# Kernel optimization log

Hardware: AMD Instinct MI355X
Metric: run time of the kernel (lower is better)

## Reference

```python
import jax, jax.numpy as jnp
import numpy as np

B, N, D = 8, 1024, 256
H = 8
DH = D // H
R = 4          # relation types 0..3; adj value 4 = no relation
FF = 1024
EPS = 1e-5


def _lin(k, fan_in, shape):
    return jax.random.normal(k, shape, jnp.float32) * (1.0 / np.sqrt(fan_in))


def setup_inputs() -> dict:
    key = jax.random.key(0)
    ks = jax.random.split(key, 16)
    src = jax.random.normal(ks[0], (B, N, D), jnp.float32)
    adj_matrix = jax.random.randint(ks[1], (B, N, N), 0, 5, dtype=jnp.int32)
    Wq = _lin(ks[2], D, (D, D)); bq = jnp.zeros((D,), jnp.float32)
    Wk = _lin(ks[3], D, (D, D)); bk = jnp.zeros((D,), jnp.float32)
    Wv = _lin(ks[4], D, (R, D, D)); bv = jnp.zeros((R, D), jnp.float32)
    Wo = _lin(ks[5], D, (D, D)); bo = jnp.zeros((D,), jnp.float32)
    W1 = _lin(ks[6], D, (D, FF)); b1 = jnp.zeros((FF,), jnp.float32)
    W2 = _lin(ks[7], FF, (FF, D)); b2 = jnp.zeros((D,), jnp.float32)
    g1 = jnp.ones((D,), jnp.float32); beta1 = jnp.zeros((D,), jnp.float32)
    g2 = jnp.ones((D,), jnp.float32); beta2 = jnp.zeros((D,), jnp.float32)
    return dict(src=src, adj_matrix=adj_matrix, Wq=Wq, bq=bq, Wk=Wk, bk=bk,
                Wv=Wv, bv=bv, Wo=Wo, bo=bo, W1=W1, b1=b1, W2=W2, b2=b2,
                g1=g1, beta1=beta1, g2=g2, beta2=beta2)


def _ln(x, g, b):
    m = x.mean(-1, keepdims=True)
    v = ((x - m) ** 2).mean(-1, keepdims=True)
    return (x - m) * jax.lax.rsqrt(v + EPS) * g + b


def reference(src, adj_matrix, Wq, bq, Wk, bk, Wv, bv, Wo, bo, W1, b1, W2, b2, g1, beta1, g2, beta2):
    Bb, Nn, Dm = src.shape
    h, dh = H, Dm // H
    q = (src @ Wq + bq).reshape(Bb, Nn, h, dh).transpose(0, 2, 1, 3)  # (B,H,N,dh)
    k = (src @ Wk + bk).reshape(Bb, Nn, h, dh).transpose(0, 2, 1, 3)
    scores = jnp.einsum('bhid,bhjd->bhij', q, k) / np.sqrt(dh)
    attn = jax.nn.softmax(scores, axis=-1)                             # (B,H,N,N)
    out = jnp.zeros_like(q)
    for r in range(Wv.shape[0]):  # small fixed relation loop, matches module
        v_r = (src @ Wv[r] + bv[r]).reshape(Bb, Nn, h, dh).transpose(0, 2, 1, 3)
        mask = (adj_matrix == r)[:, None]                              # (B,1,N,N)
        out = out + jnp.einsum('bhij,bhjd->bhid', attn * mask, v_r)
    attn_out = out.transpose(0, 2, 1, 3).reshape(Bb, Nn, Dm) @ Wo + bo
    x = _ln(src + attn_out, g1, beta1)
    ff = jax.nn.gelu(x @ W1 + b1, approximate=False) @ W2 + b2
    return _ln(x + ff, g2, beta2)
```

## Files before the change

### kernel.cpp

```cpp
#include <hip/hip_runtime.h>
#include <hip/hip_bf16.h>
#include <cmath>

constexpr int CB  = 8;
constexpr int CN  = 1024;
constexpr int CD  = 256;
constexpr int CH  = 8;
constexpr int CDH = 32;
constexpr int CR  = 4;
constexpr int CFF = 1024;
constexpr float CEPS = 1e-5f;
constexpr float CS = 0.25503480f;
constexpr size_t SZH = (size_t)CB * CH * CN * CDH;

#define MODE_QK    0
#define MODE_FFN1  2
#define MODE_VT    4

typedef float v4f __attribute__((ext_vector_type(4)));
typedef short v8s __attribute__((ext_vector_type(8)));

static __device__ __forceinline__ short f2bf(float f) {
    unsigned u = __builtin_bit_cast(unsigned, f);
    u += 0x7fff + ((u >> 16) & 1);
    return (short)(u >> 16);
}
static __device__ __forceinline__ float bf2f(short s) {
    unsigned u = ((unsigned)(unsigned short)s) << 16;
    return __builtin_bit_cast(float, u);
}
static __device__ __forceinline__ unsigned cvtpk_bf16(float lo, float hi) {
    unsigned r;
    asm("v_cvt_pk_bf16_f32 %0, %1, %2" : "=v"(r) : "v"(lo), "v"(hi));
    return r;
}

static __device__ __forceinline__ void async_copy16(const void* g, void* l) {
    __builtin_amdgcn_global_load_lds(
        (const __attribute__((address_space(1))) void*)g,
        (__attribute__((address_space(3))) void*)l, 16, 0, 0);
}


template<int BM, int BN, int MODE>
__device__ __forceinline__ void gemm_body(
    const short* __restrict__ A, const short* __restrict__ Bw,
    const float* __restrict__ biasv, void* __restrict__ dest,
    int M, int K, int Nw, int bx, int by, short* smem)
{
    constexpr int WTM = BM / 2, WTN = BN / 2;
    constexpr int TM = WTM / 16, TN = WTN / 16;
    short* As = smem;
    short* Bs = smem + 2 * BM * 32;

    const int t    = threadIdx.x;
    const int lane = t & 63;
    const int w    = t >> 6;
    const int quad = lane >> 4, l15 = lane & 15;
    const int wm = w >> 1, wn = w & 1;
    const int m0 = bx * BM, n0 = by * BN;

    const int srow = lane >> 2;
    const int scol = (lane & 3) * 8;

    v4f acc[TM][TN];
    #pragma unroll
    for (int i = 0; i < TM; ++i)
        #pragma unroll
        for (int j = 0; j < TN; ++j) acc[i][j] = (v4f){0.f, 0.f, 0.f, 0.f};

    const int NK = K >> 5;

    auto stage = [&](int buf, int kt) {
        #pragma unroll
        for (int u = 0; u < BM / 64; ++u) {
            const int e0 = (w * (BM / 64) + u) * 512;
            const int row = (e0 >> 5) + srow;
            async_copy16(A + (size_t)(m0 + row) * K + kt + scol,
                         &As[buf * BM * 32 + e0]);
        }
        #pragma unroll
        for (int u = 0; u < BN / 64; ++u) {
            const int e0 = (w * (BN / 64) + u) * 512;
            const int row = (e0 >> 5) + srow;
            async_copy16(Bw + (size_t)(n0 + row) * K + kt + scol,
                         &Bs[buf * BN * 32 + e0]);
        }
    };

    stage(0, 0);

    for (int it = 0; it < NK; ++it) {
        __syncthreads();
        if (it + 1 < NK) stage((it + 1) & 1, (it + 1) << 5);

        const int buf = it & 1;
        v8s af[TM], bfr[TN];
        #pragma unroll
        for (int i = 0; i < TM; ++i)
            af[i] = *(const v8s*)&As[buf * BM * 32 +
                                     (wm * WTM + i * 16 + l15) * 32 + quad * 8];
        #pragma unroll
        for (int j = 0; j < TN; ++j)
            bfr[j] = *(const v8s*)&Bs[buf * BN * 32 +
                                      (wn * WTN + j * 16 + l15) * 32 + quad * 8];
        #pragma unroll
        for (int i = 0; i < TM; ++i)
            #pragma unroll
            for (int j = 0; j < TN; ++j)
                acc[i][j] = __builtin_amdgcn_mfma_f32_16x16x32_bf16(
                    af[i], bfr[j], acc[i][j], 0, 0, 0);
    }

    #pragma unroll
    for (int i = 0; i < TM; ++i) {
        #pragma unroll
        for (int j = 0; j < TN; ++j) {
            const int mb = m0 + wm * WTM + i * 16 + quad * 4;
            const int n  = n0 + wn * WTN + j * 16 + l15;
            float vals[4];
            if (MODE == MODE_VT) {
                #pragma unroll
                for (int rr = 0; rr < 4; ++rr) vals[rr] = acc[i][j][rr] + biasv[mb + rr];
            } else {
                #pragma unroll
                for (int rr = 0; rr < 4; ++rr) vals[rr] = acc[i][j][rr] + biasv[n];
            }

            if (MODE == MODE_QK) {
                if (n0 < 256) {
                    #pragma unroll
                    for (int rr = 0; rr < 4; ++rr) vals[rr] *= CS;
                }
                const int b = mb >> 10, ii0 = mb & 1023;
                const int plane = n >> 8, nn = n & 255;
                const int h = nn >> 5, d = nn & 31;
                #pragma unroll
                for (int rr = 0; rr < 4; ++rr)
                    ((short*)dest)[(size_t)plane * SZH +
                        (((size_t)(b * CH + h)) * CN + ii0 + rr) * CDH + d] =
                        f2bf(vals[rr]);
            } else if (MODE == MODE_VT) {
                const int b = n >> 10, ii = n & 1023;
                const int jj = ii & 63;
                const int cc = (((jj >> 4) & 1) << 5) | (((jj >> 2) & 3) << 3) |
                               (((jj >> 5) & 1) << 2) | (jj & 3);
                const int iip = (ii & ~63) | cc;
                #pragma unroll
                for (int rr = 0; rr < 4; ++rr) {
                    const int m = mb + rr;
                    const int r2 = m >> 8, hd = m & 255;
                    const int h = hd >> 5, d = hd & 31;
                    ((short*)dest)[2 * SZH +
                        (((size_t)(r2 * 64 + b * CH + h)) * CDH + d) * CN + iip] =
                        f2bf(vals[rr]);
                }
            } else {
                #pragma unroll
                for (int rr = 0; rr < 4; ++rr) {
                    const size_t idx = (size_t)(mb + rr) * Nw + n;
                    const float xx = vals[rr];
                    const float E = exp2f(2.302217f * (xx + 0.044715f * xx * xx * xx));
                    ((short*)dest)[idx] = f2bf(xx * E / (E + 1.f));
                }
            }
        }
    }
}

template<int BM, int BN, int MODE>
__global__ __launch_bounds__(256)
void gemm_mfma(const short* __restrict__ A, const short* __restrict__ Bw,
               const float* __restrict__ biasv, void* __restrict__ dest,
               int M, int K, int Nw)
{
    extern __shared__ short smem[];
    gemm_body<BM, BN, MODE>(A, Bw, biasv, dest, M, K, Nw,
                            blockIdx.x, blockIdx.y, smem);
}

__global__ __launch_bounds__(256)
void proj_kernel(const short* __restrict__ src_bf, const short* __restrict__ wqkvT,
                 const float* __restrict__ bpack, short* __restrict__ qkv,
                 const int* __restrict__ adj, unsigned char* __restrict__ adjsel)
{
    extern __shared__ short smem[];
    const int g = blockIdx.x;
    if (g < 256) {
        gemm_body<128, 128, MODE_QK>(src_bf, wqkvT, bpack, qkv,
                                     8192, 256, 512, g >> 2, g & 3, smem);
    } else if (g < 768) {
        const int h2 = g - 256;
        gemm_body<128, 128, MODE_VT>(wqkvT + 512 * 256, src_bf, bpack + 512,
                                     qkv, 1024, 256, 8192, h2 & 7, h2 >> 3, smem);
    } else {
        const int nout = CB * CN * CN / 8;
        for (int i = (g - 768) * 256 + threadIdx.x; i < nout; i += 512 * 256) {
            const int dwi = i & 127;
            const int row = i >> 7;
            const int T   = dwi >> 3, kq = dwi & 7;
            const int j0  = T * 64 + (kq & 3) * 4 + (kq >> 2) * 16;
            const int* p = adj + (size_t)row * CN + j0;
            const int4 q0 = *(const int4*)(p);
            const int4 q1 = *(const int4*)(p + 32);
            int2 o;
            o.x = (q0.x & 0xff) | ((q0.y & 0xff) << 8) |
                  ((q0.z & 0xff) << 16) | ((q0.w & 0xff) << 24);
            o.y = (q1.x & 0xff) | ((q1.y & 0xff) << 8) |
                  ((q1.z & 0xff) << 16) | ((q1.w & 0xff) << 24);
            ((int2*)adjsel)[i] = o;
        }
    }
}

template<bool OUTF, bool OUTB, bool ADDBF>
__global__ __launch_bounds__(256)
void gemm_ln32(const short* __restrict__ A, const short* __restrict__ Bw,
               const float* __restrict__ biasv, const void* __restrict__ addp,
               const float* __restrict__ gw, const float* __restrict__ be,
               float* __restrict__ outf, short* __restrict__ outb, int K)
{
    __shared__ short As[2][16 * 32];
    __shared__ short Bs[2][256 * 32];
    __shared__ float redS[16][4], redQ[16][4];

    const int t    = threadIdx.x;
    const int lane = t & 63;
    const int w    = t >> 6;
    const int quad = lane >> 4, l15 = lane & 15;
    const int m0   = blockIdx.x * 16;

    const int srow = lane >> 2;
    const int scol = (lane & 3) * 8;

    v4f acc[4];
    #pragma unroll
    for (int j = 0; j < 4; ++j) acc[j] = (v4f){0.f, 0.f, 0.f, 0.f};

    const int NK = K >> 5;

    auto stage = [&](int buf, int kt) {
        if (t < 64)
            async_copy16(A + (size_t)(m0 + (t >> 2)) * K + kt + (t & 3) * 8,
                         &As[buf][t * 8]);
        #pragma unroll
        for (int u = 0; u < 4; ++u) {
            const int e0 = (w * 4 + u) * 512;
            async_copy16(Bw + (size_t)((e0 >> 5) + srow) * K + kt + scol,
                         &Bs[buf][e0]);
        }
    };

    stage(0, 0);

    for (int it = 0; it < NK; ++it) {
        __syncthreads();
        if (it + 1 < NK) stage((it + 1) & 1, (it + 1) << 5);

        const int buf = it & 1;
        const v8s af = *(const v8s*)&As[buf][l15 * 32 + quad * 8];
        #pragma unroll
        for (int j = 0; j < 4; ++j) {
            const v8s bfr = *(const v8s*)&Bs[buf][(w * 64 + 16 * j + l15) * 32 + quad * 8];
            acc[j] = __builtin_amdgcn_mfma_f32_16x16x32_bf16(af, bfr, acc[j], 0, 0, 0);
        }
    }

    float v[4][4];
    #pragma unroll
    for (int rr = 0; rr < 4; ++rr) {
        const int row = m0 + quad * 4 + rr;
        float s = 0.f, sq = 0.f;
        #pragma unroll
        for (int j = 0; j < 4; ++j) {
            const int n = w * 64 + 16 * j + l15;
            const size_t idx = (size_t)row * CD + n;
            const float addv = ADDBF ? bf2f(((const short*)addp)[idx])
                                     : ((const float*)addp)[idx];
            const float x = acc[j][rr] + biasv[n] + addv;
            v[rr][j] = x;
            s += x; sq += x * x;
        }
        #pragma unroll
        for (int off = 1; off < 16; off <<= 1) {
            s  += __shfl_xor(s, off);
            sq += __shfl_xor(sq, off);
        }
        if (l15 == 0) {
            redS[quad * 4 + rr][w] = s;
            redQ[quad * 4 + rr][w] = sq;
        }
    }
    __syncthreads();

    #pragma unroll
    for (int rr = 0; rr < 4; ++rr) {
        const int r16 = quad * 4 + rr;
        const int row = m0 + r16;
        const float s  = (redS[r16][0] + redS[r16][1]) + (redS[r16][2] + redS[r16][3]);
        const float sq = (redQ[r16][0] + redQ[r16][1]) + (redQ[r16][2] + redQ[r16][3]);
        const float mean = s * (1.f / CD);
        const float var  = sq * (1.f / CD) - mean * mean;
        const float rstd = rsqrtf(var + CEPS);
        #pragma unroll
        for (int j = 0; j < 4; ++j) {
            const int n = w * 64 + 16 * j + l15;
            const float y = (v[rr][j] - mean) * rstd * gw[n] + be[n];
            if (OUTF) outf[(size_t)row * CD + n] = y;
            if (OUTB) outb[(size_t)row * CD + n] = f2bf(y);
        }
    }
}

__global__ __launch_bounds__(256)
void prep(const float* __restrict__ src,
          const float* __restrict__ Wq, const float* __restrict__ Wk,
          const float* __restrict__ Wv, const float* __restrict__ Wo,
          const float* __restrict__ W1, const float* __restrict__ W2,
          const float* __restrict__ bq, const float* __restrict__ bk,
          const float* __restrict__ bv, const float* __restrict__ bo,
          const float* __restrict__ b1, const float* __restrict__ b2,
          short* __restrict__ src_bf,
          short* __restrict__ wqkvT, short* __restrict__ woT,
          short* __restrict__ w1T, short* __restrict__ w2T,
          float* __restrict__ bpack)
{
    __shared__ float tile[64][65];
    const int bx = blockIdx.x, t = threadIdx.x;
    if (bx < 2048) {
        const int i = bx * 256 + t;
        const float4 v = ((const float4*)src)[i];
        short4 o;
        o.x = f2bf(v.x); o.y = f2bf(v.y); o.z = f2bf(v.z); o.w = f2bf(v.w);
        ((short4*)src_bf)[i] = o;
    } else if (bx < 2288) {
        const int tt = bx - 2048;
        const float* S; short* D;
        int Sstride, Dstride, k0, srccol, dstrow;
        if (tt < 96) {
            const int tk = tt & 3, tn = tt >> 2;
            const int ng = tn * 64;
            Sstride = 256; Dstride = 256; k0 = tk * 64;
            dstrow = tn * 64; D = wqkvT;
            if (ng < 256)      { S = Wq; srccol = ng; }
            else if (ng < 512) { S = Wk; srccol = ng - 256; }
            else { const int r = (ng - 512) >> 8;
                   S = Wv + (size_t)r * 65536; srccol = (ng - 512) & 255; }
        } else if (tt < 112) {
            const int u = tt - 96, tk = u & 3, tn = u >> 2;
            S = Wo; Sstride = 256; D = woT; Dstride = 256;
            k0 = tk * 64; srccol = tn * 64; dstrow = tn * 64;
        } else if (tt < 176) {
            const int u = tt - 112, tk = u & 3, tn = u >> 2;
            S = W1; Sstride = 1024; D = w1T; Dstride = 256;
            k0 = tk * 64; srccol = tn * 64; dstrow = tn * 64;
        } else {
            const int u = tt - 176, tk = u & 15, tn = u >> 4;
            S = W2; Sstride = 256; D = w2T; Dstride = 1024;
            k0 = tk * 64; srccol = tn * 64; dstrow = tn * 64;
        }
        #pragma unroll
        for (int u2 = 0; u2 < 4; ++u2) {
            const int kl = (t >> 4) + u2 * 16;
            const int nl = (t & 15) * 4;
            const float4 v = *(const float4*)&S[(size_t)(k0 + kl) * Sstride + srccol + nl];
            tile[kl][nl + 0] = v.x; tile[kl][nl + 1] = v.y;
            tile[kl][nl + 2] = v.z; tile[kl][nl + 3] = v.w;
        }
        __syncthreads();
        #pragma unroll
        for (int u2 = 0; u2 < 4; ++u2) {
            const int nl = (t >> 4) + u2 * 16;
            const int kl = (t & 15) * 4;
            short4 o;
            o.x = f2bf(tile[kl + 0][nl]); o.y = f2bf(tile[kl + 1][nl]);
            o.z = f2bf(tile[kl + 2][nl]); o.w = f2bf(tile[kl + 3][nl]);
            *(short4*)&D[(size_t)(dstrow + nl) * Dstride + k0 + kl] = o;
        }
    } else {
        const int idx = (bx - 2288) * 256 + t;
        float bvv;
        if (idx < 256)       bvv = bq[idx];
        else if (idx < 512)  bvv = bk[idx - 256];
        else if (idx < 1536) bvv = bv[idx - 512];
        else if (idx < 1792) bvv = bo[idx - 1536];
        else if (idx < 2816) bvv = b1[idx - 1792];
        else                 bvv = b2[idx - 2816];
        bpack[idx] = bvv;
    }
}

__global__ __launch_bounds__(256, 4)
void attn_mfma(const short* __restrict__ qg, const short* __restrict__ kg,
               const short* __restrict__ vt, const unsigned char* __restrict__ adjsel,
               short* __restrict__ outh)
{
    __shared__ __align__(16) short vtl[2][8192];

    const int t    = threadIdx.x;
    const int lane = t & 63;
    const int w    = t >> 6;
    const int quad = lane >> 4;
    const int l15  = lane & 15;
    const int g    = blockIdx.x;
    const int b    = g & 7;
    const int h    = (g >> 3) & 7;
    const int i0   = (g >> 6) * 64;
    const int bhh  = b * CH + h;
    const size_t bh = (size_t)bhh;

    const v8s qfrag = *(const v8s*)&qg[(bh * CN + i0 + 16 * w + l15) * CDH + quad * 8];

    const short* vsrc[4];
    #pragma unroll
    for (int u = 0; u < 4; ++u) {
        const int gl = t + 256 * u;
        const int r = gl >> 8, d = (gl >> 3) & 31, gc = gl & 7;
        vsrc[u] = vt + ((size_t)(r * 64 + bhh) * CDH + d) * CN + (gc ^ (d & 7)) * 8;
    }
    const short* kbase = kg + (bh * CN + l15) * CDH + quad * 8;
    const unsigned char* abase =
        adjsel + ((size_t)(b * CN) + i0 + 16 * w + l15) * CN + quad * 8;

    v4f oacc[2];
    oacc[0] = (v4f){0.f, 0.f, 0.f, 0.f};
    oacc[1] = (v4f){0.f, 0.f, 0.f, 0.f};
    float plsum = 0.f;
    const int psw = (l15 & 7) * 8;

    #pragma unroll
    for (int u = 0; u < 4; ++u)
        async_copy16(vsrc[u], &vtl[0][(t + 256 * u) * 8]);
    v8s kpre[4];
    #pragma unroll
    for (int jb = 0; jb < 4; ++jb)
        kpre[jb] = *(const v8s*)(kbase + (16 * jb) * CDH);
    int2 apre0 = *(const int2*)(abase);
    int2 apre1 = *(const int2*)(abase + 32);

    for (int jt = 0; jt < 16; ++jt) {
        __syncthreads();
        const int p = jt & 1;

        v4f sacc[4];
        #pragma unroll
        for (int jb = 0; jb < 4; ++jb)
            sacc[jb] = __builtin_amdgcn_mfma_f32_16x16x32_bf16(
                kpre[jb], qfrag, (v4f){0.f, 0.f, 0.f, 0.f}, 0, 0, 0);

        const int2 a0 = apre0, a1 = apre1;
        const int jn = (jt + 1) & 15;
        #pragma unroll
        for (int u = 0; u < 4; ++u)
            async_copy16(vsrc[u] + jn * 64, &vtl[p ^ 1][(t + 256 * u) * 8]);
        #pragma unroll
        for (int jb = 0; jb < 4; ++jb)
            kpre[jb] = *(const v8s*)(kbase + (jn * 64 + 16 * jb) * CDH);
        apre0 = *(const int2*)(abase + jn * 64);
        apre1 = *(const int2*)(abase + jn * 64 + 32);

        float pv[4][4];
        #pragma unroll
        for (int jb = 0; jb < 4; ++jb)
            #pragma unroll
            for (int rr = 0; rr < 4; ++rr) pv[jb][rr] = exp2f(sacc[jb][rr]);
        plsum += ((pv[0][0] + pv[0][1]) + (pv[0][2] + pv[0][3]))
               + ((pv[1][0] + pv[1][1]) + (pv[1][2] + pv[1][3]))
               + ((pv[2][0] + pv[2][1]) + (pv[2][2] + pv[2][3]))
               + ((pv[3][0] + pv[3][1]) + (pv[3][2] + pv[3][3]));

        #pragma unroll
        for (int kb = 0; kb < 2; ++kb) {
            const unsigned P[4] = {
                cvtpk_bf16(pv[kb][0],     pv[kb][1]),
                cvtpk_bf16(pv[kb][2],     pv[kb][3]),
                cvtpk_bf16(pv[kb + 2][0], pv[kb + 2][1]),
                cvtpk_bf16(pv[kb + 2][2], pv[kb + 2][3])};
            const int2 aa = kb ? a1 : a0;
            const unsigned D[4] = {
                __builtin_amdgcn_perm((unsigned)aa.x, (unsigned)aa.x, 0x01010000u),
                __builtin_amdgcn_perm((unsigned)aa.x, (unsigned)aa.x, 0x03030202u),
                __builtin_amdgcn_perm((unsigned)aa.y, (unsigned)aa.y, 0x01010000u),
                __builtin_amdgcn_perm((unsigned)aa.y, (unsigned)aa.y, 0x03030202u)};
            #pragma unroll
            for (int r = 0; r < 4; ++r) {
                const unsigned tb = 0xffu << (8 * r);
                unsigned pf[4];
                #pragma unroll
                for (int u = 0; u < 4; ++u)
                    pf[u] = P[u] & __builtin_amdgcn_perm(0u, tb, D[u]);
                const v8s pfr = __builtin_bit_cast(v8s,
                    make_uint4(pf[0], pf[1], pf[2], pf[3]));
                #pragma unroll
                for (int cb = 0; cb < 2; ++cb) {
                    const v8s vfrag = *(const v8s*)&vtl[p][r * 2048 +
                        (16 * cb + l15) * 64 + (((4 * kb + quad) * 8) ^ psw)];
                    oacc[cb] = __builtin_amdgcn_mfma_f32_16x16x32_bf16(
                        pfr, vfrag, oacc[cb], 0, 0, 0);
                }
            }
        }
    }

    float plF = plsum;
    plF += __shfl_xor(plF, 16);
    plF += __shfl_xor(plF, 32);
    #pragma unroll
    for (int rr = 0; rr < 4; ++rr) {
        const float inv = 1.f / __shfl(plF, quad * 4 + rr);
        const int row = i0 + 16 * w + quad * 4 + rr;
        #pragma unroll
        for (int cb = 0; cb < 2; ++cb)
            outh[((size_t)b * CN + row) * CD + h * CDH + 16 * cb + l15] =
                f2bf(oacc[cb][rr] * inv);
    }
}

extern "C" void kernel_launch(void* const* d_in, const int* in_sizes, int n_in,
                              void* d_out, int out_size, void* d_ws, size_t ws_size,
                              hipStream_t stream)
{
    const float* src = (const float*)d_in[0];
    const int*   adj = (const int*)d_in[1];
    const float* Wq  = (const float*)d_in[2];
    const float* bq  = (const float*)d_in[3];
    const float* Wk  = (const float*)d_in[4];
    const float* bk  = (const float*)d_in[5];
    const float* Wv  = (const float*)d_in[6];
    const float* bv  = (const float*)d_in[7];
    const float* Wo  = (const float*)d_in[8];
    const float* bo  = (const float*)d_in[9];
    const float* W1  = (const float*)d_in[10];
    const float* b1  = (const float*)d_in[11];
    const float* W2  = (const float*)d_in[12];
    const float* b2  = (const float*)d_in[13];
    const float* g1  = (const float*)d_in[14];
    const float* be1 = (const float*)d_in[15];
    const float* g2  = (const float*)d_in[16];
    const float* be2 = (const float*)d_in[17];
    float* out = (float*)d_out;

    char* wsb = (char*)d_ws;
    const size_t MB = (size_t)1 << 20;

    unsigned char* adjsel = (unsigned char*)(wsb);
    short* qkv_bf = (short*)(wsb + 8 * MB);
    short* src_bf = (short*)(wsb + 32 * MB);
    short* wqkvT  = (short*)(wsb + 36 * MB);
    short* woT    = (short*)(wsb + 36 * MB + 768 * 1024);
    short* w1T    = (short*)(wsb + 36 * MB + 896 * 1024);
    short* w2T    = (short*)(wsb + 36 * MB + 1408 * 1024);
    float* bpack  = (float*)(wsb + 36 * MB + 1920 * 1024);
    short* heads_bf = (short*)(wsb + 38 * MB);
    short* x_bf   = (short*)(wsb + 32 * MB);
    short* h1_bf  = (short*)(wsb + 16 * MB);

    const int M = CB * CN;
    dim3 blk(256);

    prep<<<dim3(2300), blk, 0, stream>>>(src, Wq, Wk, Wv, Wo, W1, W2,
        bq, bk, bv, bo, b1, b2, src_bf, wqkvT, woT, w1T, w2T, bpack);

    proj_kernel<<<dim3(1280), blk, 32768, stream>>>(
        src_bf, wqkvT, bpack, qkv_bf, adj, adjsel);

    attn_mfma<<<dim3(1024), blk, 0, stream>>>(
        qkv_bf, qkv_bf + SZH, qkv_bf + 2 * SZH, adjsel, heads_bf);

    gemm_ln32<false, true, false><<<dim3(M / 16), blk, 0, stream>>>(
        heads_bf, woT, bpack + 1536, src, g1, be1, nullptr, x_bf, CD);

    gemm_mfma<128, 128, MODE_FFN1><<<dim3(M / 128, CFF / 128), blk, 32768, stream>>>(
        x_bf, w1T, bpack + 1792, h1_bf, M, CD, CFF);

    gemm_ln32<true, false, true><<<dim3(M / 16), blk, 0, stream>>>(
        h1_bf, w2T, bpack + 2816, x_bf, g2, be2, out, nullptr, CFF);
}
```

Measured before the change: 225.6 us.

## Deepen GEMM-LN K tile with swizzled LDS, split attention accumulators and batch loads

The fused GEMM+LayerNorm kernel now stages 64-wide K tiles instead of 32, using an XOR swizzle on the LDS layout to avoid bank conflicts. This halves the number of barrier-synchronised iterations at the cost of doubled shared memory. The relation-masked attention kernel hoists all V fragment LDS reads ahead of the MFMA chain and splits the output accumulators per kb to break MFMA dependency chains. It also raises wave priority around the MFMA block with s_setprio, using more registers in exchange.

```diff
diff --git a/kernel.cpp b/kernel.cpp
--- a/kernel.cpp
+++ b/kernel.cpp
@@ -220,8 +220,8 @@
                const float* __restrict__ gw, const float* __restrict__ be,
                float* __restrict__ outf, short* __restrict__ outb, int K)
 {
-    __shared__ short As[2][16 * 32];
-    __shared__ short Bs[2][256 * 32];
+    __shared__ short As[2][16 * 64];
+    __shared__ short Bs[2][256 * 64];
     __shared__ float redS[16][4], redQ[16][4];
 
     const int t    = threadIdx.x;
@@ -229,25 +229,26 @@
     const int w    = t >> 6;
     const int quad = lane >> 4, l15 = lane & 15;
     const int m0   = blockIdx.x * 16;
-
-    const int srow = lane >> 2;
-    const int scol = (lane & 3) * 8;
+    const int xsw  = l15 & 7;
 
     v4f acc[4];
     #pragma unroll
     for (int j = 0; j < 4; ++j) acc[j] = (v4f){0.f, 0.f, 0.f, 0.f};
 
-    const int NK = K >> 5;
+    const int NK = K >> 6;
 
     auto stage = [&](int buf, int kt) {
-        if (t < 64)
-            async_copy16(A + (size_t)(m0 + (t >> 2)) * K + kt + (t & 3) * 8,
+        if (t < 128) {
+            const int row = t >> 3, gc = t & 7;
+            async_copy16(A + (size_t)(m0 + row) * K + kt + ((gc ^ (row & 7)) * 8),
                          &As[buf][t * 8]);
-        #pragma unroll
-        for (int u = 0; u < 4; ++u) {
-            const int e0 = (w * 4 + u) * 512;
-            async_copy16(Bw + (size_t)((e0 >> 5) + srow) * K + kt + scol,
-                         &Bs[buf][e0]);
+        }
+        #pragma unroll
+        for (int u = 0; u < 8; ++u) {
+            const int gl = t + 256 * u;
+            const int row = gl >> 3, gc = gl & 7;
+            async_copy16(Bw + (size_t)row * K + kt + ((gc ^ (row & 7)) * 8),
+                         &Bs[buf][gl * 8]);
         }
     };
 
@@ -255,14 +256,18 @@
 
     for (int it = 0; it < NK; ++it) {
         __syncthreads();
-        if (it + 1 < NK) stage((it + 1) & 1, (it + 1) << 5);
+        if (it + 1 < NK) stage((it + 1) & 1, (it + 1) << 6);
 
         const int buf = it & 1;
-        const v8s af = *(const v8s*)&As[buf][l15 * 32 + quad * 8];
-        #pragma unroll
-        for (int j = 0; j < 4; ++j) {
-            const v8s bfr = *(const v8s*)&Bs[buf][(w * 64 + 16 * j + l15) * 32 + quad * 8];
-            acc[j] = __builtin_amdgcn_mfma_f32_16x16x32_bf16(af, bfr, acc[j], 0, 0, 0);
+        #pragma unroll
+        for (int half = 0; half < 2; ++half) {
+            const int gr = (quad + 4 * half) ^ xsw;
+            const v8s af = *(const v8s*)&As[buf][l15 * 64 + gr * 8];
+            #pragma unroll
+            for (int j = 0; j < 4; ++j) {
+                const v8s bfr = *(const v8s*)&Bs[buf][(w * 64 + 16 * j + l15) * 64 + gr * 8];
+                acc[j] = __builtin_amdgcn_mfma_f32_16x16x32_bf16(af, bfr, acc[j], 0, 0, 0);
+            }
         }
     }
 
@@ -422,9 +427,11 @@
     const unsigned char* abase =
         adjsel + ((size_t)(b * CN) + i0 + 16 * w + l15) * CN + quad * 8;
 
-    v4f oacc[2];
-    oacc[0] = (v4f){0.f, 0.f, 0.f, 0.f};
-    oacc[1] = (v4f){0.f, 0.f, 0.f, 0.f};
+    v4f oacc[2][2];
+    #pragma unroll
+    for (int cb = 0; cb < 2; ++cb)
+        #pragma unroll
+        for (int kb = 0; kb < 2; ++kb) oacc[cb][kb] = (v4f){0.f, 0.f, 0.f, 0.f};
     float plsum = 0.f;
     const int psw = (l15 & 7) * 8;
 
@@ -471,6 +478,14 @@
 
         #pragma unroll
         for (int kb = 0; kb < 2; ++kb) {
+            v8s vf[4][2];
+            #pragma unroll
+            for (int r = 0; r < 4; ++r)
+                #pragma unroll
+                for (int cb = 0; cb < 2; ++cb)
+                    vf[r][cb] = *(const v8s*)&vtl[p][r * 2048 +
+                        (16 * cb + l15) * 64 + (((4 * kb + quad) * 8) ^ psw)];
+
             const unsigned P[4] = {
                 cvtpk_bf16(pv[kb][0],     pv[kb][1]),
                 cvtpk_bf16(pv[kb][2],     pv[kb][3]),
@@ -482,26 +497,31 @@
                 __builtin_amdgcn_perm((unsigned)aa.x, (unsigned)aa.x, 0x03030202u),
                 __builtin_amdgcn_perm((unsigned)aa.y, (unsigned)aa.y, 0x01010000u),
                 __builtin_amdgcn_perm((unsigned)aa.y, (unsigned)aa.y, 0x03030202u)};
+            unsigned pfm[4][4];
             #pragma unroll
             for (int r = 0; r < 4; ++r) {
                 const unsigned tb = 0xffu << (8 * r);
-                unsigned pf[4];
                 #pragma unroll
                 for (int u = 0; u < 4; ++u)
-                    pf[u] = P[u] & __builtin_amdgcn_perm(0u, tb, D[u]);
+                    pfm[r][u] = P[u] & __builtin_amdgcn_perm(0u, tb, D[u]);
+            }
+            __builtin_amdgcn_s_setprio(1);
+            #pragma unroll
+            for (int r = 0; r < 4; ++r) {
                 const v8s pfr = __builtin_bit_cast(v8s,
-                    make_uint4(pf[0], pf[1], pf[2], pf[3]));
-                #pragma unroll
-                for (int cb = 0; cb < 2; ++cb) {
-                    const v8s vfrag = *(const v8s*)&vtl[p][r * 2048 +
-                        (16 * cb + l15) * 64 + (((4 * kb + quad) * 8) ^ psw)];
-                    oacc[cb] = __builtin_amdgcn_mfma_f32_16x16x32_bf16(
-                        pfr, vfrag, oacc[cb], 0, 0, 0);
-                }
+                    make_uint4(pfm[r][0], pfm[r][1], pfm[r][2], pfm[r][3]));
+                #pragma unroll
+                for (int cb = 0; cb < 2; ++cb)
+                    oacc[cb][kb] = __builtin_amdgcn_mfma_f32_16x16x32_bf16(
+                        pfr, vf[r][cb], oacc[cb][kb], 0, 0, 0);
             }
-        }
-    }
-
+            __builtin_amdgcn_s_setprio(0);
+        }
+    }
+
+    v4f ofin[2];
+    ofin[0] = oacc[0][0] + oacc[0][1];
+    ofin[1] = oacc[1][0] + oacc[1][1];
     float plF = plsum;
     plF += __shfl_xor(plF, 16);
     plF += __shfl_xor(plF, 32);
@@ -512,7 +532,7 @@
         #pragma unroll
         for (int cb = 0; cb < 2; ++cb)
             outh[((size_t)b * CN + row) * CD + h * CDH + 16 * cb + l15] =
-                f2bf(oacc[cb][rr] * inv);
+                f2bf(ofin[cb][rr] * inv);
     }
 }
 
```

Measured after the change: 216.8 us. 1.04x faster.
